# Optimization experiments

Hardware: AMD Instinct MI355X
Metric: run time of the kernel (lower is better)

## Reference

```python
import jax, jax.numpy as jnp
import numpy as np

ALPHA = 0.2        # LeakyReLU slope for attention scores (init arg alpha)
MLP_ALPHA = 0.01   # torch nn.LeakyReLU default slope in aftermlp
EPS = 1e-5         # nn.LayerNorm default eps


def leaky(x, a):
    return jnp.where(x >= 0, x, a * x)


def setup_inputs() -> dict:
    key = jax.random.key(0)
    ks = jax.random.split(key, 12)
    B, N, FIN, FOUT, K = 4, 4096, 256, 256, 64
    s = 0.05
    return {
        "h": jax.random.normal(ks[0], (B, N, FIN), jnp.float32),
        "adj": jax.random.uniform(ks[1], (B, N, N), jnp.float32),
        "W": jax.random.normal(ks[2], (FIN, FOUT), jnp.float32) * s,
        "a": jax.random.normal(ks[3], (FOUT, 1), jnp.float32) * s,
        "ln_g": jnp.ones((FOUT,), jnp.float32),
        "ln_b": jnp.zeros((FOUT,), jnp.float32),
        "W1": jax.random.normal(ks[4], (FOUT, FOUT), jnp.float32) * s,
        "b1": jnp.zeros((FOUT,), jnp.float32),
        "W2": jax.random.normal(ks[5], (FOUT, FOUT), jnp.float32) * s,
        "b2": jnp.zeros((FOUT,), jnp.float32),
        "W3": jax.random.normal(ks[6], (FOUT, FOUT), jnp.float32) * s,
        "b3": jnp.zeros((FOUT,), jnp.float32),
        "k": K,
    }


def reference(h, adj, W, a, ln_g, ln_b, W1, b1, W2, b2, W3, b3, k):
    # Wh: [B, N, F]
    Wh = h @ W
    B, N, Fd = Wh.shape
    C = N // k
    Whc = Wh.reshape(B, C, k, Fd)                       # [B, C, k, F]
    # a_input[b,c,i,j] = Wh[b,c,i]  =>  e[b,c,i,j] = leaky(Wh[b,c,i] . a)
    e = leaky(jnp.squeeze(Whc @ a, -1), ALPHA)          # [B, C, k]
    # block-diagonal chunks of adj: [B, C, k, k]
    idx = jnp.arange(C)
    blocks = adj.reshape(B, C, k, C, k)[:, idx, :, idx, :]  # [C, B, k, k]
    blocks = jnp.transpose(blocks, (1, 0, 2, 3))            # [B, C, k, k]
    scores = jax.nn.softmax(blocks * e[..., :, None], axis=-1)  # [B, C, k, k]
    out = jnp.einsum('bcij,bcjf->bcif', scores, Whc)    # [B, C, k, F]
    # aftermlp: Linear -> LeakyReLU(0.01) -> Linear -> LeakyReLU(0.01) -> Linear
    y = leaky(out @ W1 + b1, MLP_ALPHA)
    y = leaky(y @ W2 + b2, MLP_ALPHA)
    y = y @ W3 + b3
    # residual + LayerNorm over last dim
    z = y + out
    mu = jnp.mean(z, axis=-1, keepdims=True)
    var = jnp.var(z, axis=-1, keepdims=True)
    z = (z - mu) / jnp.sqrt(var + EPS) * ln_g + ln_b
    return z.reshape(B, N, Fd)
```

## Files before the change

kernel.cpp:

```cpp
#include <hip/hip_runtime.h>

typedef __bf16 bf16;
typedef __bf16 bf16x4 __attribute__((ext_vector_type(4)));
typedef __bf16 bf16x8 __attribute__((ext_vector_type(8)));
typedef float  f32x4  __attribute__((ext_vector_type(4)));

#define ALPHA 0.2f
#define MLP_ALPHA 0.01f
#define LN_EPS 1e-5f

constexpr int Bb = 4;
constexpr int Nn = 4096;
constexpr int Ff = 256;
constexpr int Kk = 64;
constexpr int Cc = 64;

__device__ __forceinline__ f32x4 MFMA(bf16x8 a, bf16x8 b, f32x4 c) {
  return __builtin_amdgcn_mfma_f32_16x16x32_bf16(a, b, c, 0, 0, 0);
}
__device__ __forceinline__ bf16x4 pack4(f32x4 v) {
  bf16x4 r; r[0]=(bf16)v[0]; r[1]=(bf16)v[1]; r[2]=(bf16)v[2]; r[3]=(bf16)v[3]; return r;
}
__device__ __forceinline__ int swz512(int i, int inrow) { return i*512 + (inrow ^ ((i & 15) << 4)); }
__device__ __forceinline__ int swz128(int f, int inrow) { return f*128 + (inrow ^ ((f & 7) << 4)); }

__global__ __launch_bounds__(256) void prep_weights(
    const float* __restrict__ W0, const float* __restrict__ W1,
    const float* __restrict__ W2, const float* __restrict__ W3,
    const float* __restrict__ a_vec,
    bf16* __restrict__ outw, float* __restrict__ wa)
{
  if (blockIdx.x == 128) {
    int k = threadIdx.x;
    const float* row = W0 + k * Ff;
    float s = 0.f;
    for (int j = 0; j < Ff; j += 4) {
      f32x4 wv = *(const f32x4*)(row + j);
      f32x4 av = *(const f32x4*)(a_vec + j);
      s += wv[0]*av[0] + wv[1]*av[1] + wv[2]*av[2] + wv[3]*av[3];
    }
    wa[k] = s;
    return;
  }
  int t = blockIdx.x * 256 + threadIdx.x;
  int l = t & 63, nt = (t >> 6) & 15, kt = (t >> 10) & 7, mat = t >> 13;
  const float* src = (mat==0) ? W0 : (mat==1) ? W1 : (mat==2) ? W2 : W3;
  int n  = nt*16 + (l & 15);
  int k0 = kt*32 + (l >> 4)*8;
  bf16x8 v;
  #pragma unroll
  for (int jj = 0; jj < 8; ++jj) v[jj] = (bf16)src[(k0 + jj)*Ff + n];
  *(bf16x8*)(outw + (size_t)t * 8) = v;
}

__global__ __launch_bounds__(1024, 4) void gat_mfma(
    const float* __restrict__ h,   const float* __restrict__ adj,
    const float* __restrict__ gln, const float* __restrict__ bln,
    const float* __restrict__ b1,  const float* __restrict__ b2,
    const float* __restrict__ b3,
    const bf16* __restrict__ wfrag, const float* __restrict__ wa,
    float* __restrict__ out)
{
  __shared__ bf16 hbs[Kk * Ff];
  __shared__ bf16 bufA[Ff * Kk];
  __shared__ bf16 bufB[Kk * Ff];
  __shared__ bf16 sShi[Kk * Kk];
  __shared__ bf16 sSlo[Kk * Kk];
  __shared__ float evec[Kk];
  __shared__ float lnS[Kk * 8], lnQ[Kk * 8];

  const int t = threadIdx.x, l = t & 63, w = t >> 6, g = l >> 4, li = l & 15;
  const int wf = w & 7;
  const int wi = w >> 3;
  const int bc = blockIdx.x, b = bc >> 6, c = bc & 63;
  const size_t rbase = (size_t)b * Nn + c * Kk;

  float adjv[4];
  #pragma unroll
  for (int rr = 0; rr < 4; ++rr)
    adjv[rr] = adj[(rbase + w*4 + rr) * Nn + (size_t)c*Kk + l];

  {
    const int i  = t >> 4;
    const int k0 = (t & 15) * 16;
    const float* hp = h + (rbase + i) * Ff + k0;
    float p = 0.f;
    #pragma unroll
    for (int u = 0; u < 2; ++u) {
      f32x4 h0 = *(const f32x4*)(hp + u*8);
      f32x4 h1 = *(const f32x4*)(hp + u*8 + 4);
      f32x4 w0 = *(const f32x4*)(wa + k0 + u*8);
      f32x4 w1 = *(const f32x4*)(wa + k0 + u*8 + 4);
      p += h0[0]*w0[0] + h0[1]*w0[1] + h0[2]*w0[2] + h0[3]*w0[3]
         + h1[0]*w1[0] + h1[1]*w1[1] + h1[2]*w1[2] + h1[3]*w1[3];
      bf16x8 v;
      #pragma unroll
      for (int d = 0; d < 4; ++d) { v[d] = (bf16)h0[d]; v[4+d] = (bf16)h1[d]; }
      *(bf16x8*)((char*)hbs + swz512(i, (k0 + u*8)*2)) = v;
    }
    p += __shfl_xor(p, 1); p += __shfl_xor(p, 2);
    p += __shfl_xor(p, 4); p += __shfl_xor(p, 8);
    if ((t & 15) == 0) evec[i] = (p >= 0.f) ? p : ALPHA * p;
  }
  __syncthreads();

  #pragma unroll
  for (int rr = 0; rr < 4; ++rr) {
    int i = w*4 + rr;
    float x = adjv[rr] * evec[i];
    float m = x;
    #pragma unroll
    for (int off = 32; off; off >>= 1) m = fmaxf(m, __shfl_xor(m, off));
    float pe = __expf(x - m);
    float s = pe;
    #pragma unroll
    for (int off = 32; off; off >>= 1) s += __shfl_xor(s, off);
    float sv = pe / s;
    bf16 hi = (bf16)sv;
    *(bf16*)((char*)sShi + swz128(i, l*2)) = hi;
    *(bf16*)((char*)sSlo + swz128(i, l*2)) = (bf16)(sv - (float)hi);
  }

  f32x4 acc1[2][2];
  #pragma unroll
  for (int q = 0; q < 2; ++q)
    #pragma unroll
    for (int rt = 0; rt < 2; ++rt) acc1[q][rt] = (f32x4){0.f,0.f,0.f,0.f};
  #pragma unroll
  for (int kt = 0; kt < 8; ++kt) {
    bf16x8 af[2];
    #pragma unroll
    for (int rt = 0; rt < 2; ++rt) {
      int i = (wi*2 + rt)*16 + li;
      af[rt] = *(const bf16x8*)((const char*)hbs + swz512(i, (kt*32 + g*8)*2));
    }
    #pragma unroll
    for (int q = 0; q < 2; ++q) {
      bf16x8 bfr = *(const bf16x8*)(wfrag + (((size_t)kt*16 + (wf*2 + q))*64 + l)*8);
      #pragma unroll
      for (int rt = 0; rt < 2; ++rt) acc1[q][rt] = MFMA(af[rt], bfr, acc1[q][rt]);
    }
  }
  #pragma unroll
  for (int q = 0; q < 2; ++q) {
    int f = (wf*2 + q)*16 + li;
    #pragma unroll
    for (int rt = 0; rt < 2; ++rt) {
      int j0 = (wi*2 + rt)*16 + g*4;
      *(bf16x4*)((char*)bufA + swz128(f, j0*2)) = pack4(acc1[q][rt]);
    }
  }
  __syncthreads();

  f32x4 xr[2][2];
  #pragma unroll
  for (int nt = 0; nt < 2; ++nt)
    #pragma unroll
    for (int r = 0; r < 2; ++r) xr[nt][r] = (f32x4){0.f,0.f,0.f,0.f};
  #pragma unroll
  for (int kt = 0; kt < 2; ++kt) {
    int koff = (kt*32 + g*8)*2;
    bf16x8 af[2], bfrH[2], bfrL[2];
    #pragma unroll
    for (int r = 0; r < 2; ++r) {
      int f = (wf*2 + r)*16 + li;
      af[r] = *(const bf16x8*)((const char*)bufA + swz128(f, koff));
    }
    #pragma unroll
    for (int nt = 0; nt < 2; ++nt) {
      int i = (wi*2 + nt)*16 + li;
      bfrH[nt] = *(const bf16x8*)((const char*)sShi + swz128(i, koff));
      bfrL[nt] = *(const bf16x8*)((const char*)sSlo + swz128(i, koff));
    }
    #pragma unroll
    for (int nt = 0; nt < 2; ++nt)
      #pragma unroll
      for (int r = 0; r < 2; ++r) {
        xr[nt][r] = MFMA(af[r], bfrL[nt], xr[nt][r]);
        xr[nt][r] = MFMA(af[r], bfrH[nt], xr[nt][r]);
      }
  }
  #pragma unroll
  for (int nt = 0; nt < 2; ++nt) {
    int i = (wi*2 + nt)*16 + li;
    #pragma unroll
    for (int r = 0; r < 2; ++r) {
      int f0 = (wf*2 + r)*16 + g*4;
      *(bf16x4*)((char*)bufB + swz512(i, f0*2)) = pack4(xr[nt][r]);
    }
  }
  __syncthreads();

  f32x4 acc3[2][2];
  #pragma unroll
  for (int stage = 0; stage < 3; ++stage) {
    const bf16* inB = (stage == 1) ? bufA : bufB;
    #pragma unroll
    for (int nt = 0; nt < 2; ++nt)
      #pragma unroll
      for (int r = 0; r < 2; ++r) acc3[nt][r] = (f32x4){0.f,0.f,0.f,0.f};
    #pragma unroll
    for (int kt = 0; kt < 8; ++kt) {
      bf16x8 af[2], bfr[2];
      #pragma unroll
      for (int r = 0; r < 2; ++r)
        af[r] = *(const bf16x8*)(wfrag + ((((size_t)(stage+1)*8 + kt)*16 + (wf*2 + r))*64 + l)*8);
      #pragma unroll
      for (int nt = 0; nt < 2; ++nt) {
        int i = (wi*2 + nt)*16 + li;
        bfr[nt] = *(const bf16x8*)((const char*)inB + swz512(i, (kt*32 + g*8)*2));
      }
      #pragma unroll
      for (int nt = 0; nt < 2; ++nt)
        #pragma unroll
        for (int r = 0; r < 2; ++r)
          acc3[nt][r] = MFMA(af[r], bfr[nt], acc3[nt][r]);
    }
    if (stage == 2) break;
    __syncthreads();
    const float* bias = (stage == 0) ? b1 : b2;
    bf16* outB = (stage == 0) ? bufA : bufB;
    #pragma unroll
    for (int nt = 0; nt < 2; ++nt) {
      int i = (wi*2 + nt)*16 + li;
      #pragma unroll
      for (int r = 0; r < 2; ++r) {
        f32x4 v;
        #pragma unroll
        for (int e = 0; e < 4; ++e) {
          float x = acc3[nt][r][e] + bias[(wf*2 + r)*16 + g*4 + e];
          v[e] = (x >= 0.f) ? x : MLP_ALPHA * x;
        }
        int f0 = (wf*2 + r)*16 + g*4;
        *(bf16x4*)((char*)outB + swz512(i, f0*2)) = pack4(v);
      }
    }
    __syncthreads();
  }

  {
    float bv[2][4], gv[2][4], btv[2][4];
    #pragma unroll
    for (int r = 0; r < 2; ++r)
      #pragma unroll
      for (int e = 0; e < 4; ++e) {
        int f = (wf*2 + r)*16 + g*4 + e;
        bv[r][e] = b3[f]; gv[r][e] = gln[f]; btv[r][e] = bln[f];
      }
    #pragma unroll
    for (int nt = 0; nt < 2; ++nt) {
      float s = 0.f, qq = 0.f;
      #pragma unroll
      for (int r = 0; r < 2; ++r)
        #pragma unroll
        for (int e = 0; e < 4; ++e) {
          float z = acc3[nt][r][e] + bv[r][e] + xr[nt][r][e];
          acc3[nt][r][e] = z;
          s += z; qq += z*z;
        }
      s  += __shfl_xor(s, 16);  s  += __shfl_xor(s, 32);
      qq += __shfl_xor(qq, 16); qq += __shfl_xor(qq, 32);
      if (g == 0) {
        int i = (wi*2 + nt)*16 + li;
        lnS[i*8 + wf] = s;
        lnQ[i*8 + wf] = qq;
      }
    }
    __syncthreads();
    #pragma unroll
    for (int nt = 0; nt < 2; ++nt) {
      int i = (wi*2 + nt)*16 + li;
      f32x4 s0 = *(const f32x4*)&lnS[i*8];
      f32x4 s1 = *(const f32x4*)&lnS[i*8 + 4];
      f32x4 q0 = *(const f32x4*)&lnQ[i*8];
      f32x4 q1 = *(const f32x4*)&lnQ[i*8 + 4];
      float s  = s0[0]+s0[1]+s0[2]+s0[3]+s1[0]+s1[1]+s1[2]+s1[3];
      float qq = q0[0]+q0[1]+q0[2]+q0[3]+q1[0]+q1[1]+q1[2]+q1[3];
      float mu  = s * (1.f/256.f);
      float var = qq * (1.f/256.f) - mu*mu;
      float rs  = rsqrtf(var + LN_EPS);
      #pragma unroll
      for (int r = 0; r < 2; ++r) {
        float4 o;
        o.x = (acc3[nt][r][0] - mu)*rs*gv[r][0] + btv[r][0];
        o.y = (acc3[nt][r][1] - mu)*rs*gv[r][1] + btv[r][1];
        o.z = (acc3[nt][r][2] - mu)*rs*gv[r][2] + btv[r][2];
        o.w = (acc3[nt][r][3] - mu)*rs*gv[r][3] + btv[r][3];
        *(float4*)&out[(rbase + i)*Ff + (wf*2 + r)*16 + g*4] = o;
      }
    }
  }
}

extern "C" void kernel_launch(void* const* d_in, const int* in_sizes, int n_in,
                              void* d_out, int out_size, void* d_ws, size_t ws_size,
                              hipStream_t stream) {
  (void)in_sizes; (void)n_in; (void)out_size; (void)ws_size;
  bf16*  wfrag = (bf16*)d_ws;
  float* wa    = (float*)((char*)d_ws + 512*1024);
  prep_weights<<<dim3(129), dim3(256), 0, stream>>>(
      (const float*)d_in[2], (const float*)d_in[6],
      (const float*)d_in[8], (const float*)d_in[10],
      (const float*)d_in[3], wfrag, wa);
  gat_mfma<<<dim3(Bb * Cc), dim3(1024), 0, stream>>>(
      (const float*)d_in[0],  (const float*)d_in[1],
      (const float*)d_in[4],  (const float*)d_in[5],
      (const float*)d_in[7],  (const float*)d_in[9],  (const float*)d_in[11],
      wfrag, wa, (float*)d_out);
}
```

Before: 36.07 us.

## Split h staging to overlap Wh MFMAs, drop bf16 hi/lo score split

The h row load and bf16 staging are split into two halves. The first four k-tiles of the h@W MFMA run before the second half is converted and the attention vector is finished, so global loads overlap with matrix work. The softmax scores are now stored as a single bf16 value instead of a hi/lo pair, which halves the score LDS footprint and the MFMAs in the aggregation step at some cost in precision. One __syncthreads in the MLP stage loop is also removed, since the input and output buffers of each stage are distinct.

```diff
diff --git a/kernel.cpp b/kernel.cpp
--- a/kernel.cpp
+++ b/kernel.cpp
@@ -64,8 +64,7 @@
   __shared__ bf16 hbs[Kk * Ff];
   __shared__ bf16 bufA[Ff * Kk];
   __shared__ bf16 bufB[Kk * Ff];
-  __shared__ bf16 sShi[Kk * Kk];
-  __shared__ bf16 sSlo[Kk * Kk];
+  __shared__ bf16 sS[Kk * Kk];
   __shared__ float evec[Kk];
   __shared__ float lnS[Kk * 8], lnQ[Kk * 8];
 
@@ -80,27 +79,62 @@
   for (int rr = 0; rr < 4; ++rr)
     adjv[rr] = adj[(rbase + w*4 + rr) * Nn + (size_t)c*Kk + l];
 
+  const int i16 = t >> 4;
+  const int s16 = t & 15;
+  const int cA  = s16 * 8;
+  const float* hpA = h + (rbase + i16) * Ff + cA;
+  float pA;
   {
-    const int i  = t >> 4;
-    const int k0 = (t & 15) * 16;
-    const float* hp = h + (rbase + i) * Ff + k0;
-    float p = 0.f;
-    #pragma unroll
-    for (int u = 0; u < 2; ++u) {
-      f32x4 h0 = *(const f32x4*)(hp + u*8);
-      f32x4 h1 = *(const f32x4*)(hp + u*8 + 4);
-      f32x4 w0 = *(const f32x4*)(wa + k0 + u*8);
-      f32x4 w1 = *(const f32x4*)(wa + k0 + u*8 + 4);
-      p += h0[0]*w0[0] + h0[1]*w0[1] + h0[2]*w0[2] + h0[3]*w0[3]
-         + h1[0]*w1[0] + h1[1]*w1[1] + h1[2]*w1[2] + h1[3]*w1[3];
-      bf16x8 v;
-      #pragma unroll
-      for (int d = 0; d < 4; ++d) { v[d] = (bf16)h0[d]; v[4+d] = (bf16)h1[d]; }
-      *(bf16x8*)((char*)hbs + swz512(i, (k0 + u*8)*2)) = v;
-    }
+    f32x4 h0 = *(const f32x4*)(hpA);
+    f32x4 h1 = *(const f32x4*)(hpA + 4);
+    f32x4 w0 = *(const f32x4*)(wa + cA);
+    f32x4 w1 = *(const f32x4*)(wa + cA + 4);
+    pA = h0[0]*w0[0] + h0[1]*w0[1] + h0[2]*w0[2] + h0[3]*w0[3]
+       + h1[0]*w1[0] + h1[1]*w1[1] + h1[2]*w1[2] + h1[3]*w1[3];
+    bf16x8 v;
+    #pragma unroll
+    for (int d = 0; d < 4; ++d) { v[d] = (bf16)h0[d]; v[4+d] = (bf16)h1[d]; }
+    *(bf16x8*)((char*)hbs + swz512(i16, cA*2)) = v;
+  }
+  __syncthreads();
+
+  f32x4 h0b = *(const f32x4*)(hpA + 128);
+  f32x4 h1b = *(const f32x4*)(hpA + 132);
+
+  f32x4 acc1[2][2];
+  #pragma unroll
+  for (int q = 0; q < 2; ++q)
+    #pragma unroll
+    for (int rt = 0; rt < 2; ++rt) acc1[q][rt] = (f32x4){0.f,0.f,0.f,0.f};
+  #pragma unroll
+  for (int kt = 0; kt < 4; ++kt) {
+    bf16x8 af[2];
+    #pragma unroll
+    for (int rt = 0; rt < 2; ++rt) {
+      int i = (wi*2 + rt)*16 + li;
+      af[rt] = *(const bf16x8*)((const char*)hbs + swz512(i, (kt*32 + g*8)*2));
+    }
+    #pragma unroll
+    for (int q = 0; q < 2; ++q) {
+      bf16x8 bfr = *(const bf16x8*)(wfrag + (((size_t)kt*16 + (wf*2 + q))*64 + l)*8);
+      #pragma unroll
+      for (int rt = 0; rt < 2; ++rt) acc1[q][rt] = MFMA(af[rt], bfr, acc1[q][rt]);
+    }
+  }
+
+  {
+    f32x4 w0 = *(const f32x4*)(wa + 128 + cA);
+    f32x4 w1 = *(const f32x4*)(wa + 132 + cA);
+    float p = pA
+      + h0b[0]*w0[0] + h0b[1]*w0[1] + h0b[2]*w0[2] + h0b[3]*w0[3]
+      + h1b[0]*w1[0] + h1b[1]*w1[1] + h1b[2]*w1[2] + h1b[3]*w1[3];
+    bf16x8 v;
+    #pragma unroll
+    for (int d = 0; d < 4; ++d) { v[d] = (bf16)h0b[d]; v[4+d] = (bf16)h1b[d]; }
+    *(bf16x8*)((char*)hbs + swz512(i16, (128 + cA)*2)) = v;
     p += __shfl_xor(p, 1); p += __shfl_xor(p, 2);
     p += __shfl_xor(p, 4); p += __shfl_xor(p, 8);
-    if ((t & 15) == 0) evec[i] = (p >= 0.f) ? p : ALPHA * p;
+    if (s16 == 0) evec[i16] = (p >= 0.f) ? p : ALPHA * p;
   }
   __syncthreads();
 
@@ -115,19 +149,11 @@
     float s = pe;
     #pragma unroll
     for (int off = 32; off; off >>= 1) s += __shfl_xor(s, off);
-    float sv = pe / s;
-    bf16 hi = (bf16)sv;
-    *(bf16*)((char*)sShi + swz128(i, l*2)) = hi;
-    *(bf16*)((char*)sSlo + swz128(i, l*2)) = (bf16)(sv - (float)hi);
-  }
-
-  f32x4 acc1[2][2];
-  #pragma unroll
-  for (int q = 0; q < 2; ++q)
-    #pragma unroll
-    for (int rt = 0; rt < 2; ++rt) acc1[q][rt] = (f32x4){0.f,0.f,0.f,0.f};
-  #pragma unroll
-  for (int kt = 0; kt < 8; ++kt) {
+    *(bf16*)((char*)sS + swz128(i, l*2)) = (bf16)(pe / s);
+  }
+
+  #pragma unroll
+  for (int kt = 4; kt < 8; ++kt) {
     bf16x8 af[2];
     #pragma unroll
     for (int rt = 0; rt < 2; ++rt) {
@@ -160,7 +186,7 @@
   #pragma unroll
   for (int kt = 0; kt < 2; ++kt) {
     int koff = (kt*32 + g*8)*2;
-    bf16x8 af[2], bfrH[2], bfrL[2];
+    bf16x8 af[2], bfr[2];
     #pragma unroll
     for (int r = 0; r < 2; ++r) {
       int f = (wf*2 + r)*16 + li;
@@ -169,16 +195,13 @@
     #pragma unroll
     for (int nt = 0; nt < 2; ++nt) {
       int i = (wi*2 + nt)*16 + li;
-      bfrH[nt] = *(const bf16x8*)((const char*)sShi + swz128(i, koff));
-      bfrL[nt] = *(const bf16x8*)((const char*)sSlo + swz128(i, koff));
+      bfr[nt] = *(const bf16x8*)((const char*)sS + swz128(i, koff));
     }
     #pragma unroll
     for (int nt = 0; nt < 2; ++nt)
       #pragma unroll
-      for (int r = 0; r < 2; ++r) {
-        xr[nt][r] = MFMA(af[r], bfrL[nt], xr[nt][r]);
-        xr[nt][r] = MFMA(af[r], bfrH[nt], xr[nt][r]);
-      }
+      for (int r = 0; r < 2; ++r)
+        xr[nt][r] = MFMA(af[r], bfr[nt], xr[nt][r]);
   }
   #pragma unroll
   for (int nt = 0; nt < 2; ++nt) {
@@ -217,7 +240,6 @@
           acc3[nt][r] = MFMA(af[r], bfr[nt], acc3[nt][r]);
     }
     if (stage == 2) break;
-    __syncthreads();
     const float* bias = (stage == 0) ? b1 : b2;
     bf16* outB = (stage == 0) ? bufA : bufB;
     #pragma unroll
```

After: 36.31 us. About the same (+0.7%).

## Split Wh projection into separate wide kernel and drop split-bf16 softmax MFMAs

Applied to the files above, without the earlier changes.

Moves the h@W projection and attention-vector dot into a new 1024-block kernel that writes a bf16 transposed Wh image and e-vector to workspace. The main kernel then loads that image into shared memory instead of computing it. The main kernel launches only 256 blocks, so the projection now runs with more parallelism. The change also drops the hi/lo bf16 split of the softmax scores, halving the MFMAs in the aggregation, and removes one barrier in the MLP stages. In exchange it adds a launch and a workspace round trip, loses some score precision, and the removed barrier may introduce a read/write race on the shared buffers.

```diff
diff --git a/kernel.cpp b/kernel.cpp
--- a/kernel.cpp
+++ b/kernel.cpp
@@ -14,6 +14,10 @@
 constexpr int Ff = 256;
 constexpr int Kk = 64;
 constexpr int Cc = 64;
+
+constexpr size_t WS_WA   = 524288;
+constexpr size_t WS_EVEC = 525312;
+constexpr size_t WS_IMG  = 1048576;
 
 __device__ __forceinline__ f32x4 MFMA(bf16x8 a, bf16x8 b, f32x4 c) {
   return __builtin_amdgcn_mfma_f32_16x16x32_bf16(a, b, c, 0, 0, 0);
@@ -53,20 +57,68 @@
   *(bf16x8*)(outw + (size_t)t * 8) = v;
 }
 
-__global__ __launch_bounds__(1024, 4) void gat_mfma(
-    const float* __restrict__ h,   const float* __restrict__ adj,
+__global__ __launch_bounds__(256, 4) void wh_e(
+    const float* __restrict__ h, const bf16* __restrict__ wfrag,
+    const float* __restrict__ wa, bf16* __restrict__ img, float* __restrict__ ews)
+{
+  const int t = threadIdx.x, l = t & 63, w = t >> 6, g = l >> 4, li = l & 15;
+  const int rb = blockIdx.x * 16;
+
+  {
+    const int r = t >> 4, s16 = t & 15;
+    const float* hp = h + (size_t)(rb + r) * Ff + s16 * 16;
+    float p = 0.f;
+    #pragma unroll
+    for (int u = 0; u < 2; ++u) {
+      f32x4 h0 = *(const f32x4*)(hp + u*8);
+      f32x4 h1 = *(const f32x4*)(hp + u*8 + 4);
+      f32x4 w0 = *(const f32x4*)(wa + s16*16 + u*8);
+      f32x4 w1 = *(const f32x4*)(wa + s16*16 + u*8 + 4);
+      p += h0[0]*w0[0]+h0[1]*w0[1]+h0[2]*w0[2]+h0[3]*w0[3]
+         + h1[0]*w1[0]+h1[1]*w1[1]+h1[2]*w1[2]+h1[3]*w1[3];
+    }
+    p += __shfl_xor(p, 1); p += __shfl_xor(p, 2);
+    p += __shfl_xor(p, 4); p += __shfl_xor(p, 8);
+    if (s16 == 0) ews[rb + r] = (p >= 0.f) ? p : ALPHA * p;
+  }
+
+  f32x4 acc[4];
+  #pragma unroll
+  for (int q = 0; q < 4; ++q) acc[q] = (f32x4){0.f,0.f,0.f,0.f};
+  const float* ap0 = h + (size_t)(rb + li) * Ff + g*8;
+  #pragma unroll
+  for (int kt = 0; kt < 8; ++kt) {
+    f32x4 a0 = *(const f32x4*)(ap0 + kt*32);
+    f32x4 a1 = *(const f32x4*)(ap0 + kt*32 + 4);
+    bf16x8 af;
+    #pragma unroll
+    for (int d = 0; d < 4; ++d) { af[d] = (bf16)a0[d]; af[4+d] = (bf16)a1[d]; }
+    #pragma unroll
+    for (int q = 0; q < 4; ++q) {
+      bf16x8 bfr = *(const bf16x8*)(wfrag + (((size_t)kt*16 + (w*4 + q))*64 + l)*8);
+      acc[q] = MFMA(af, bfr, acc[q]);
+    }
+  }
+  bf16* ib = img + (size_t)(blockIdx.x >> 2) * (Ff * Kk);
+  const int j0 = (blockIdx.x & 3)*16 + g*4;
+  #pragma unroll
+  for (int q = 0; q < 4; ++q) {
+    int f = (w*4 + q)*16 + li;
+    *(bf16x4*)(ib + f*64 + j0) = pack4(acc[q]);
+  }
+}
+
+__global__ __launch_bounds__(1024, 4) void gat2(
+    const float* __restrict__ adj,
     const float* __restrict__ gln, const float* __restrict__ bln,
     const float* __restrict__ b1,  const float* __restrict__ b2,
     const float* __restrict__ b3,
-    const bf16* __restrict__ wfrag, const float* __restrict__ wa,
-    float* __restrict__ out)
+    const bf16* __restrict__ wfrag, const bf16* __restrict__ img,
+    const float* __restrict__ ews,  float* __restrict__ out)
 {
-  __shared__ bf16 hbs[Kk * Ff];
-  __shared__ bf16 bufA[Ff * Kk];
-  __shared__ bf16 bufB[Kk * Ff];
-  __shared__ bf16 sShi[Kk * Kk];
-  __shared__ bf16 sSlo[Kk * Kk];
-  __shared__ float evec[Kk];
+  __shared__ __align__(16) bf16 bufA[Ff * Kk];
+  __shared__ __align__(16) bf16 bufB[Kk * Ff];
+  __shared__ __align__(16) bf16 sS[Kk * Kk];
   __shared__ float lnS[Kk * 8], lnQ[Kk * 8];
 
   const int t = threadIdx.x, l = t & 63, w = t >> 6, g = l >> 4, li = l & 15;
@@ -80,34 +132,15 @@
   for (int rr = 0; rr < 4; ++rr)
     adjv[rr] = adj[(rbase + w*4 + rr) * Nn + (size_t)c*Kk + l];
 
-  {
-    const int i  = t >> 4;
-    const int k0 = (t & 15) * 16;
-    const float* hp = h + (rbase + i) * Ff + k0;
-    float p = 0.f;
-    #pragma unroll
-    for (int u = 0; u < 2; ++u) {
-      f32x4 h0 = *(const f32x4*)(hp + u*8);
-      f32x4 h1 = *(const f32x4*)(hp + u*8 + 4);
-      f32x4 w0 = *(const f32x4*)(wa + k0 + u*8);
-      f32x4 w1 = *(const f32x4*)(wa + k0 + u*8 + 4);
-      p += h0[0]*w0[0] + h0[1]*w0[1] + h0[2]*w0[2] + h0[3]*w0[3]
-         + h1[0]*w1[0] + h1[1]*w1[1] + h1[2]*w1[2] + h1[3]*w1[3];
-      bf16x8 v;
-      #pragma unroll
-      for (int d = 0; d < 4; ++d) { v[d] = (bf16)h0[d]; v[4+d] = (bf16)h1[d]; }
-      *(bf16x8*)((char*)hbs + swz512(i, (k0 + u*8)*2)) = v;
-    }
-    p += __shfl_xor(p, 1); p += __shfl_xor(p, 2);
-    p += __shfl_xor(p, 4); p += __shfl_xor(p, 8);
-    if ((t & 15) == 0) evec[i] = (p >= 0.f) ? p : ALPHA * p;
-  }
-  __syncthreads();
+  const uint4* src = (const uint4*)(img + (size_t)bc * (Ff * Kk));
+  uint4 im0 = src[t];
+  uint4 im1 = src[t + 1024];
 
   #pragma unroll
   for (int rr = 0; rr < 4; ++rr) {
     int i = w*4 + rr;
-    float x = adjv[rr] * evec[i];
+    float ev = ews[bc*64 + i];
+    float x = adjv[rr] * ev;
     float m = x;
     #pragma unroll
     for (int off = 32; off; off >>= 1) m = fmaxf(m, __shfl_xor(m, off));
@@ -115,40 +148,16 @@
     float s = pe;
     #pragma unroll
     for (int off = 32; off; off >>= 1) s += __shfl_xor(s, off);
-    float sv = pe / s;
-    bf16 hi = (bf16)sv;
-    *(bf16*)((char*)sShi + swz128(i, l*2)) = hi;
-    *(bf16*)((char*)sSlo + swz128(i, l*2)) = (bf16)(sv - (float)hi);
-  }
-
-  f32x4 acc1[2][2];
-  #pragma unroll
-  for (int q = 0; q < 2; ++q)
-    #pragma unroll
-    for (int rt = 0; rt < 2; ++rt) acc1[q][rt] = (f32x4){0.f,0.f,0.f,0.f};
-  #pragma unroll
-  for (int kt = 0; kt < 8; ++kt) {
-    bf16x8 af[2];
-    #pragma unroll
-    for (int rt = 0; rt < 2; ++rt) {
-      int i = (wi*2 + rt)*16 + li;
-      af[rt] = *(const bf16x8*)((const char*)hbs + swz512(i, (kt*32 + g*8)*2));
-    }
-    #pragma unroll
-    for (int q = 0; q < 2; ++q) {
-      bf16x8 bfr = *(const bf16x8*)(wfrag + (((size_t)kt*16 + (wf*2 + q))*64 + l)*8);
-      #pragma unroll
-      for (int rt = 0; rt < 2; ++rt) acc1[q][rt] = MFMA(af[rt], bfr, acc1[q][rt]);
-    }
-  }
-  #pragma unroll
-  for (int q = 0; q < 2; ++q) {
-    int f = (wf*2 + q)*16 + li;
-    #pragma unroll
-    for (int rt = 0; rt < 2; ++rt) {
-      int j0 = (wi*2 + rt)*16 + g*4;
-      *(bf16x4*)((char*)bufA + swz128(f, j0*2)) = pack4(acc1[q][rt]);
-    }
+    *(bf16*)((char*)sS + swz128(i, l*2)) = (bf16)(pe / s);
+  }
+
+  {
+    int off = t * 16;
+    int f = off >> 7, ir = off & 127;
+    *(uint4*)((char*)bufA + f*128 + (ir ^ ((f & 7) << 4))) = im0;
+    off = (t + 1024) * 16;
+    f = off >> 7; ir = off & 127;
+    *(uint4*)((char*)bufA + f*128 + (ir ^ ((f & 7) << 4))) = im1;
   }
   __syncthreads();
 
@@ -160,7 +169,7 @@
   #pragma unroll
   for (int kt = 0; kt < 2; ++kt) {
     int koff = (kt*32 + g*8)*2;
-    bf16x8 af[2], bfrH[2], bfrL[2];
+    bf16x8 af[2], bfr[2];
     #pragma unroll
     for (int r = 0; r < 2; ++r) {
       int f = (wf*2 + r)*16 + li;
@@ -169,16 +178,13 @@
     #pragma unroll
     for (int nt = 0; nt < 2; ++nt) {
       int i = (wi*2 + nt)*16 + li;
-      bfrH[nt] = *(const bf16x8*)((const char*)sShi + swz128(i, koff));
-      bfrL[nt] = *(const bf16x8*)((const char*)sSlo + swz128(i, koff));
+      bfr[nt] = *(const bf16x8*)((const char*)sS + swz128(i, koff));
     }
     #pragma unroll
     for (int nt = 0; nt < 2; ++nt)
       #pragma unroll
-      for (int r = 0; r < 2; ++r) {
-        xr[nt][r] = MFMA(af[r], bfrL[nt], xr[nt][r]);
-        xr[nt][r] = MFMA(af[r], bfrH[nt], xr[nt][r]);
-      }
+      for (int r = 0; r < 2; ++r)
+        xr[nt][r] = MFMA(af[r], bfr[nt], xr[nt][r]);
   }
   #pragma unroll
   for (int nt = 0; nt < 2; ++nt) {
@@ -217,7 +223,6 @@
           acc3[nt][r] = MFMA(af[r], bfr[nt], acc3[nt][r]);
     }
     if (stage == 2) break;
-    __syncthreads();
     const float* bias = (stage == 0) ? b1 : b2;
     bf16* outB = (stage == 0) ? bufA : bufB;
     #pragma unroll
@@ -297,14 +302,18 @@
                               hipStream_t stream) {
   (void)in_sizes; (void)n_in; (void)out_size; (void)ws_size;
   bf16*  wfrag = (bf16*)d_ws;
-  float* wa    = (float*)((char*)d_ws + 512*1024);
+  float* wa    = (float*)((char*)d_ws + WS_WA);
+  float* ews   = (float*)((char*)d_ws + WS_EVEC);
+  bf16*  img   = (bf16*)((char*)d_ws + WS_IMG);
   prep_weights<<<dim3(129), dim3(256), 0, stream>>>(
       (const float*)d_in[2], (const float*)d_in[6],
       (const float*)d_in[8], (const float*)d_in[10],
       (const float*)d_in[3], wfrag, wa);
-  gat_mfma<<<dim3(Bb * Cc), dim3(1024), 0, stream>>>(
-      (const float*)d_in[0],  (const float*)d_in[1],
+  wh_e<<<dim3(1024), dim3(256), 0, stream>>>(
+      (const float*)d_in[0], wfrag, wa, img, ews);
+  gat2<<<dim3(Bb * Cc), dim3(1024), 0, stream>>>(
+      (const float*)d_in[1],
       (const float*)d_in[4],  (const float*)d_in[5],
       (const float*)d_in[7],  (const float*)d_in[9],  (const float*)d_in[11],
-      wfrag, wa, (float*)d_out);
-}
+      wfrag, img, ews, (float*)d_out);
+}
```

Measured after the change: 49.19 us. +36.4%, slower.
